# Kernel optimization log

Hardware: AMD Instinct MI355X
Metric: run time of the kernel (lower is better)

The kernel has to match this reference:

```python
import jax, jax.numpy as jnp
import numpy as np

DIM = 1024
N_HEADS = 16
HEAD_DIM = DIM // N_HEADS
COND_DIM = 1024
MLP_RATIO = 4
B = 8
L = 1024  # per-sequence length (equal lengths -> T = B*L packed tokens)
T = B * L
EPS = 1e-5


def setup_inputs() -> dict:
    key = jax.random.key(0)
    ks = jax.random.split(key, 16)
    s = 0.02
    # rotary tables: [max_pos, head_dim//2]
    inv_freq = 1.0 / (10000.0 ** (jnp.arange(0, HEAD_DIM, 2, dtype=jnp.float32) / HEAD_DIM))
    t = jnp.arange(L, dtype=jnp.float32)
    freqs = t[:, None] * inv_freq[None, :]  # [L, HEAD_DIM//2]
    return {
        "x": jax.random.normal(ks[0], (T, DIM), jnp.float32),
        "lengths": jnp.full((B,), L, dtype=jnp.int64),
        "offsets": jnp.arange(B, dtype=jnp.int64) * L,
        "cos": jnp.cos(freqs),
        "sin": jnp.sin(freqs),
        "positions": jnp.tile(jnp.arange(L, dtype=jnp.int64), B),
        "c": jax.random.normal(ks[1], (B, COND_DIM), jnp.float32),
        "ln1_w": jnp.ones((DIM,), jnp.float32),
        "Wq": jax.random.normal(ks[2], (DIM, DIM), jnp.float32) * s,
        "Wk": jax.random.normal(ks[3], (DIM, DIM), jnp.float32) * s,
        "Wv": jax.random.normal(ks[4], (DIM, DIM), jnp.float32) * s,
        "Wo": jax.random.normal(ks[5], (DIM, DIM), jnp.float32) * s,
        "ln2_w": jnp.ones((DIM,), jnp.float32),
        "W1": jax.random.normal(ks[6], (DIM, MLP_RATIO * DIM), jnp.float32) * s,
        "b1": jnp.zeros((MLP_RATIO * DIM,), jnp.float32),
        "W2": jax.random.normal(ks[7], (MLP_RATIO * DIM, DIM), jnp.float32) * s,
        "b2": jnp.zeros((DIM,), jnp.float32),
        "ada_w": jax.random.normal(ks[8], (COND_DIM, 6 * DIM), jnp.float32) * s,
        "ada_b": jnp.zeros((6 * DIM,), jnp.float32),
    }


def _layer_norm(x, w):
    # LayerNorm with weight only (no bias), as in the torch module
    mu = jnp.mean(x, axis=-1, keepdims=True)
    var = jnp.mean(jnp.square(x - mu), axis=-1, keepdims=True)
    return (x - mu) * jax.lax.rsqrt(var + EPS) * w


def _rope(q, k, cos, sin, positions):
    # q, k: [T, H, D]; cos/sin: [max_pos, D//2]; half-split RoPE
    c = cos[positions][:, None, :]  # [T, 1, D//2]
    s = sin[positions][:, None, :]
    def rot(x):
        x1, x2 = jnp.split(x, 2, axis=-1)
        return jnp.concatenate([x1 * c - x2 * s, x2 * c + x1 * s], axis=-1)
    return rot(q), rot(k)


def reference(x, lengths, offsets, cos, sin, positions, c,
              ln1_w, Wq, Wk, Wv, Wo, ln2_w, W1, b1, W2, b2, ada_w, ada_b):
    # adaLN modulation: [B, 6*DIM] -> six [B, DIM]
    ada = c @ ada_w + ada_b
    sh_msa, sc_msa, g_msa, sh_mlp, sc_mlp, g_mlp = jnp.split(ada, 6, axis=-1)
    # per-token gather via seq_ids (equal lengths -> repeat each row L times)
    seq_ids = jnp.repeat(jnp.arange(B), L)  # = repeat_interleave(arange(B), lengths)
    sh_msa_t, sc_msa_t, g_msa_t = sh_msa[seq_ids], sc_msa[seq_ids], g_msa[seq_ids]
    sh_mlp_t, sc_mlp_t, g_mlp_t = sh_mlp[seq_ids], sc_mlp[seq_ids], g_mlp[seq_ids]

    x_skip = x
    h = _layer_norm(x, ln1_w) * (1.0 + sc_msa_t) + sh_msa_t
    q = (h @ Wq).reshape(T, N_HEADS, HEAD_DIM)
    k = (h @ Wk).reshape(T, N_HEADS, HEAD_DIM)
    v = (h @ Wv).reshape(T, N_HEADS, HEAD_DIM)
    q, k = _rope(q, k, cos, sin, positions)

    # intra-sequence-only attention: with equal lengths the block-diagonal
    # score_mod mask is exactly per-sequence attention -> reshape to [B, L, H, D]
    qb = q.reshape(B, L, N_HEADS, HEAD_DIM)
    kb = k.reshape(B, L, N_HEADS, HEAD_DIM)
    vb = v.reshape(B, L, N_HEADS, HEAD_DIM)
    scores = jnp.einsum('blhd,bmhd->bhlm', qb, kb) / jnp.sqrt(jnp.float32(HEAD_DIM))
    probs = jax.nn.softmax(scores, axis=-1)
    attn = jnp.einsum('bhlm,bmhd->blhd', probs, vb).reshape(T, DIM)

    x = x_skip + g_msa_t * (attn @ Wo)  # dropout p is identity in eval mode

    h2 = _layer_norm(x, ln2_w) * (1.0 + sc_mlp_t) + sh_mlp_t
    mlp = jax.nn.gelu(h2 @ W1 + b1, approximate=True) @ W2 + b2
    return x + g_mlp_t * mlp
```

## Files before the change

kernel.cpp:

```cpp
#include <hip/hip_runtime.h>

typedef unsigned short u16;
typedef __attribute__((ext_vector_type(8))) short short8;
typedef __attribute__((ext_vector_type(4))) float f32x4;
typedef __attribute__((ext_vector_type(4))) unsigned uint4v;

__device__ __forceinline__ float bf2f(u16 u){
  unsigned v = ((unsigned)u) << 16;
  return __builtin_bit_cast(float, v);
}
__device__ __forceinline__ u16 f2bf(float f){
  unsigned u = __builtin_bit_cast(unsigned, f);
  u += 0x7fff + ((u >> 16) & 1);
  return (u16)(u >> 16);
}
__device__ __forceinline__ unsigned packbf(float lo, float hi){
  return ((unsigned)f2bf(hi) << 16) | (unsigned)f2bf(lo);
}
__device__ __forceinline__ void async16(const void* g, void* l){
  __builtin_amdgcn_global_load_lds((const __attribute__((address_space(1))) void*)g,
                                   (__attribute__((address_space(3))) void*)l, 16, 0, 0);
}
#define VMW(n) asm volatile("s_waitcnt vmcnt(" #n ")" ::: "memory")

__global__ __launch_bounds__(256) void ada_partial(
    const float* __restrict__ c, const float* __restrict__ aw,
    float* __restrict__ part){
  int n  = blockIdx.x*256 + threadIdx.x;
  int b  = blockIdx.y;
  int kc = blockIdx.z;
  const float* cr  = c + b*1024 + kc*128;
  const float* awp = aw + (size_t)(kc*128)*6144 + n;
  float acc = 0.f;
#pragma unroll 8
  for (int k = 0; k < 128; ++k)
    acc += cr[k] * awp[(size_t)k*6144];
  part[(size_t)(kc*8 + b)*6144 + n] = acc;
}

__global__ __launch_bounds__(256) void ada_reduce(
    const float* __restrict__ part, const float* __restrict__ ab,
    float* __restrict__ ada){
  int idx = blockIdx.x*256 + threadIdx.x;
  int n = idx % 6144;
  float acc = ab[n];
#pragma unroll
  for (int kc = 0; kc < 8; ++kc)
    acc += part[(size_t)kc*49152 + idx];
  ada[idx] = acc;
}

__global__ __launch_bounds__(256) void transpose_cast(
    const float* __restrict__ src, u16* __restrict__ dst, int K, int N){
  __shared__ float t[64][65];
  int n0 = blockIdx.x*64, k0 = blockIdx.y*64;
  int tid = threadIdx.x;
  int cc = tid & 63, r4 = tid >> 6;
#pragma unroll 4
  for (int it = 0; it < 16; ++it){
    int r = it*4 + r4;
    t[r][cc] = src[(size_t)(k0 + r)*N + n0 + cc];
  }
  __syncthreads();
#pragma unroll 4
  for (int it = 0; it < 16; ++it){
    int r = it*4 + r4;
    dst[(size_t)(n0 + r)*K + k0 + cc] = f2bf(t[cc][r]);
  }
}

__global__ __launch_bounds__(256) void ln_mod(
    const float* __restrict__ x, u16* __restrict__ out,
    const float* __restrict__ w, const float* __restrict__ ada,
    int shift_off, int scale_off){
  int t = blockIdx.x, tid = threadIdx.x;
  const float* xr = x + (size_t)t*1024;
  float v[4]; float s = 0.f, ss = 0.f;
#pragma unroll
  for (int i = 0; i < 4; ++i){ v[i] = xr[tid + i*256]; s += v[i]; ss += v[i]*v[i]; }
  for (int d = 1; d < 64; d <<= 1){ s += __shfl_xor(s, d); ss += __shfl_xor(ss, d); }
  __shared__ float red[8];
  int wv = tid >> 6;
  if ((tid & 63) == 0){ red[wv] = s; red[4+wv] = ss; }
  __syncthreads();
  s = red[0]+red[1]+red[2]+red[3];
  ss = red[4]+red[5]+red[6]+red[7];
  float mu = s * (1.f/1024.f);
  float var = ss * (1.f/1024.f) - mu*mu;
  float rs = rsqrtf(var + 1e-5f);
  int b = t >> 10;
  const float* sh = ada + b*6144 + shift_off;
  const float* sc = ada + b*6144 + scale_off;
#pragma unroll
  for (int i = 0; i < 4; ++i){
    int cidx = tid + i*256;
    float hh = (v[i]-mu)*rs*w[cidx]*(1.f + sc[cidx]) + sh[cidx];
    out[(size_t)t*1024 + cidx] = f2bf(hh);
  }
}

template<int EPI>
__device__ __forceinline__ void gemm_epi(
    void* Cout, int m, int n, int N, int m_off, float v,
    const float* e0, const float* e1, const float* e2){
  if (EPI == 0){
    ((u16*)Cout)[(size_t)m*N + n] = f2bf(v);
  } else if (EPI == 1){
    const int b = (m + m_off) >> 10;
    float g = e1[b*6144 + 2048 + n];
    ((float*)Cout)[(size_t)m*N + n] = e0[(size_t)m*N + n] + g*v;
  } else if (EPI == 2){
    float xx = v + e0[n];
    float u = xx*(1.5957691216f + 0.07135481626f*xx*xx);
    ((u16*)Cout)[(size_t)m*N + n] = f2bf(xx / (1.f + __expf(-u)));
  } else {
    const int b = (m + m_off) >> 10;
    float g = e1[b*6144 + 5120 + n];
    ((float*)Cout)[(size_t)m*N + n] = e2[(size_t)m*N + n] + g*(v + e0[n]);
  }
}

template<int EPI>
__global__ __launch_bounds__(512, 2) void gemm_bt(
    const u16* __restrict__ A, const u16* __restrict__ Bt,
    void* __restrict__ Cout, int M, int N, int K, int m_off,
    const float* __restrict__ e0, const float* __restrict__ e1,
    const float* __restrict__ e2){
  __shared__ u16 lds[65536];
  const int tid = threadIdx.x;
  const int wv = tid >> 6, lane = tid & 63;
  const int quad = lane >> 4, ln = lane & 15;
  const int wr = wv >> 2, wc = wv & 3;
  const int n0 = blockIdx.x*256, m0 = blockIdx.y*256;
  const int nt = K >> 5;

  const int swslot = (lane & 3) ^ ((lane >> 3) & 3);
  const u16* Ap = A  + (size_t)(m0 + wv*16 + (lane>>2))*K + swslot*8;
  const u16* Bp = Bt + (size_t)(n0 + wv*16 + (lane>>2))*K + swslot*8;
  const size_t hstep = (size_t)128*K;
  u16* lw = lds + wv*512;

  f32x4 acc[8][4] = {};

#pragma unroll
  for (int tau = 0; tau < 3; ++tau){
    u16* d = lw + tau*16384;
    async16(Ap + (size_t)tau*32,         d);
    async16(Ap + hstep + (size_t)tau*32, d + 4096);
    async16(Bp + (size_t)tau*32,         d + 8192);
    async16(Bp + hstep + (size_t)tau*32, d + 12288);
  }
  VMW(8);
  __builtin_amdgcn_s_barrier();

  const int rsw = (quad ^ ((ln >> 1) & 3))*8;
  const u16* Ar = lds + (wr*128 + ln)*32 + rsw;
  const u16* Br = lds + 8192 + (wc*64 + ln)*32 + rsw;

  for (int t = 0; t < nt; ++t){
    const int bo = (t & 3)*16384;
    short8 bfr[4], af[4];
#pragma unroll
    for (int j = 0; j < 4; ++j) bfr[j] = *(const short8*)(Br + bo + j*512);
#pragma unroll
    for (int i = 0; i < 4; ++i) af[i]  = *(const short8*)(Ar + bo + i*512);
    if (t + 3 < nt){
      u16* d = lw + ((t+3)&3)*16384;
      async16(Ap + (size_t)(t+3)*32,         d);
      async16(Ap + hstep + (size_t)(t+3)*32, d + 4096);
    }
    __builtin_amdgcn_s_barrier();
    __builtin_amdgcn_s_setprio(1);
#pragma unroll
    for (int i = 0; i < 4; ++i)
#pragma unroll
      for (int j = 0; j < 4; ++j)
        acc[i][j] = __builtin_amdgcn_mfma_f32_16x16x32_bf16(af[i], bfr[j], acc[i][j], 0, 0, 0);
    __builtin_amdgcn_s_setprio(0);
    __builtin_amdgcn_s_barrier();
#pragma unroll
    for (int i = 0; i < 4; ++i) af[i] = *(const short8*)(Ar + bo + 2048 + i*512);
    if (t + 3 < nt){
      u16* d = lw + ((t+3)&3)*16384;
      async16(Bp + (size_t)(t+3)*32,         d + 8192);
      async16(Bp + hstep + (size_t)(t+3)*32, d + 12288);
    }
    __builtin_amdgcn_s_barrier();
    __builtin_amdgcn_s_setprio(1);
#pragma unroll
    for (int i = 0; i < 4; ++i)
#pragma unroll
      for (int j = 0; j < 4; ++j)
        acc[4+i][j] = __builtin_amdgcn_mfma_f32_16x16x32_bf16(af[i], bfr[j], acc[4+i][j], 0, 0, 0);
    __builtin_amdgcn_s_setprio(0);
    if (t + 4 <= nt)      VMW(8);
    else if (t + 3 == nt) VMW(4);
    else if (t + 2 == nt) VMW(0);
    __builtin_amdgcn_s_barrier();
  }

  const int mB = m0 + wr*128 + quad*4;
  const int nB = n0 + wc*64 + ln;
#pragma unroll
  for (int i = 0; i < 8; ++i)
#pragma unroll
    for (int r = 0; r < 4; ++r)
#pragma unroll
      for (int j = 0; j < 4; ++j)
        gemm_epi<EPI>(Cout, mB + i*16 + r, nB + j*16, N, m_off, acc[i][j][r], e0, e1, e2);
}

template<int EPI>
__global__ __launch_bounds__(256, 2) void gemm_bt128(
    const u16* __restrict__ A, const u16* __restrict__ Bt,
    void* __restrict__ Cout, int M, int N, int K, int m_off,
    const float* __restrict__ e0, const float* __restrict__ e1,
    const float* __restrict__ e2){
  __shared__ u16 lds[32768];
  const int tid = threadIdx.x;
  const int wv = tid >> 6, lane = tid & 63;
  const int quad = lane >> 4, ln = lane & 15;
  const int wr = wv >> 1, wc = wv & 1;
  const int n0 = blockIdx.x*128, m0 = blockIdx.y*128;
  const int nt = K >> 5;

  const int swslot = (lane & 3) ^ ((lane >> 3) & 3);
  const u16* Ap = A  + (size_t)(m0 + wv*16 + (lane>>2))*K + swslot*8;
  const u16* Bp = Bt + (size_t)(n0 + wv*16 + (lane>>2))*K + swslot*8;
  const size_t hstep = (size_t)64*K;
  u16* lw = lds + wv*512;

  f32x4 acc[4][4] = {};

#pragma unroll
  for (int tau = 0; tau < 3; ++tau){
    u16* d = lw + tau*8192;
    async16(Ap + (size_t)tau*32,         d);
    async16(Ap + hstep + (size_t)tau*32, d + 2048);
    async16(Bp + (size_t)tau*32,         d + 4096);
    async16(Bp + hstep + (size_t)tau*32, d + 6144);
  }
  VMW(8);
  __builtin_amdgcn_s_barrier();

  const int rsw = (quad ^ ((ln >> 1) & 3))*8;
  const u16* Ar = lds + (wr*64 + ln)*32 + rsw;
  const u16* Br = lds + 4096 + (wc*64 + ln)*32 + rsw;

  for (int t = 0; t < nt; ++t){
    const int bo = (t & 3)*8192;
    short8 bfr[4], af[2];
#pragma unroll
    for (int j = 0; j < 4; ++j) bfr[j] = *(const short8*)(Br + bo + j*512);
#pragma unroll
    for (int i = 0; i < 2; ++i) af[i]  = *(const short8*)(Ar + bo + i*512);
    if (t + 3 < nt){
      u16* d = lw + ((t+3)&3)*8192;
      async16(Ap + (size_t)(t+3)*32,         d);
      async16(Ap + hstep + (size_t)(t+3)*32, d + 2048);
    }
    __builtin_amdgcn_s_barrier();
    __builtin_amdgcn_s_setprio(1);
#pragma unroll
    for (int i = 0; i < 2; ++i)
#pragma unroll
      for (int j = 0; j < 4; ++j)
        acc[i][j] = __builtin_amdgcn_mfma_f32_16x16x32_bf16(af[i], bfr[j], acc[i][j], 0, 0, 0);
    __builtin_amdgcn_s_setprio(0);
    __builtin_amdgcn_s_barrier();
#pragma unroll
    for (int i = 0; i < 2; ++i) af[i] = *(const short8*)(Ar + bo + 1024 + i*512);
    if (t + 3 < nt){
      u16* d = lw + ((t+3)&3)*8192;
      async16(Bp + (size_t)(t+3)*32,         d + 4096);
      async16(Bp + hstep + (size_t)(t+3)*32, d + 6144);
    }
    __builtin_amdgcn_s_barrier();
    __builtin_amdgcn_s_setprio(1);
#pragma unroll
    for (int i = 0; i < 2; ++i)
#pragma unroll
      for (int j = 0; j < 4; ++j)
        acc[2+i][j] = __builtin_amdgcn_mfma_f32_16x16x32_bf16(af[i], bfr[j], acc[2+i][j], 0, 0, 0);
    __builtin_amdgcn_s_setprio(0);
    if (t + 4 <= nt)      VMW(8);
    else if (t + 3 == nt) VMW(4);
    else if (t + 2 == nt) VMW(0);
    __builtin_amdgcn_s_barrier();
  }

  const int mB = m0 + wr*64 + quad*4;
  const int nB = n0 + wc*64 + ln;
#pragma unroll
  for (int i = 0; i < 4; ++i)
#pragma unroll
    for (int r = 0; r < 4; ++r)
#pragma unroll
      for (int j = 0; j < 4; ++j)
        gemm_epi<EPI>(Cout, mB + i*16 + r, nB + j*16, N, m_off, acc[i][j][r], e0, e1, e2);
}

__global__ __launch_bounds__(256) void rope_pack(
    const u16* __restrict__ qkv, const float* __restrict__ cosT,
    const float* __restrict__ sinT, u16* __restrict__ qp,
    u16* __restrict__ kp, u16* __restrict__ vt){
  int blk = blockIdx.x;
  int lt = blk & 15, h = (blk >> 4) & 15, b = blk >> 8;
  int l0 = lt*64;
  int bh = b*16 + h;
  __shared__ u16 vl[64][68];
  int tid = threadIdx.x;
  size_t tile_base = (size_t)bh*65536 + (size_t)lt*4096;
#pragma unroll 4
  for (int it = 0; it < 16; ++it){
    int idx = it*256 + tid;
    int r = idx >> 6, d = idx & 63;
    int t = b*1024 + l0 + r;
    int pos = l0 + r;
    const u16* row = qkv + (size_t)t*3072 + h*64;
    float qv = bf2f(row[d]), kv = bf2f(row[1024+d]);
    float qo, ko;
    if (d < 32){
      float cs = cosT[pos*32 + d], sn = sinT[pos*32 + d];
      qo = qv*cs - bf2f(row[d+32])*sn;
      ko = kv*cs - bf2f(row[1024+d+32])*sn;
    } else {
      int dd = d - 32;
      float cs = cosT[pos*32 + dd], sn = sinT[pos*32 + dd];
      qo = qv*cs + bf2f(row[d-32])*sn;
      ko = kv*cs + bf2f(row[1024+d-32])*sn;
    }
    qp[((size_t)bh*1024 + l0 + r)*64 + d] = f2bf(qo*0.125f);
    kp[tile_base + (d>>5)*2048 + r*32 + (d&31)] = f2bf(ko);
    vl[d][r] = row[2048 + d];
  }
  __syncthreads();
#pragma unroll 4
  for (int it = 0; it < 16; ++it){
    int idx = it*256 + tid;
    int d = idx >> 6, cc = idx & 63;
    vt[tile_base + (cc>>5)*2048 + d*32 + (cc&31)] = vl[d][cc];
  }
}

__global__ __launch_bounds__(256) void attn_kernel(
    const u16* __restrict__ qp, const u16* __restrict__ kp,
    const u16* __restrict__ vtp, u16* __restrict__ ao){
  __shared__ u16 Kb[4096];
  __shared__ u16 Vb[4096];
  int tid = threadIdx.x, w = tid >> 6, lane = tid & 63;
  int quad = lane >> 4, ln = lane & 15;
  int bh = blockIdx.x >> 4, qb = blockIdx.x & 15;
  int h = bh & 15, b = bh >> 4;
  const u16* Q  = qp  + ((size_t)bh*1024 + qb*64 + w*16)*64;
  const u16* Kg = kp  + (size_t)bh*65536;
  const u16* Vg = vtp + (size_t)bh*65536;
  short8 qf0 = *(const short8*)(Q + ln*64 + quad*8);
  short8 qf1 = *(const short8*)(Q + ln*64 + 32 + quad*8);
  f32x4 o[4] = {};
  float m = -3e38f, l = 0.f;
  for (int kt = 0; kt < 16; ++kt){
    const u16* ktg = Kg + kt*4096 + lane*8;
    const u16* vtg = Vg + kt*4096 + lane*8;
    async16(ktg + (w*2+0)*512, Kb + (w*2+0)*512);
    async16(ktg + (w*2+1)*512, Kb + (w*2+1)*512);
    async16(vtg + (w*2+0)*512, Vb + (w*2+0)*512);
    async16(vtg + (w*2+1)*512, Vb + (w*2+1)*512);
    __syncthreads();
    f32x4 zz = {0.f, 0.f, 0.f, 0.f};
    f32x4 st[4];
#pragma unroll
    for (int c = 0; c < 4; ++c){
      short8 k0 = *(const short8*)(Kb +        (c*16 + ln)*32 + quad*8);
      short8 k1 = *(const short8*)(Kb + 2048 + (c*16 + ln)*32 + quad*8);
      st[c] = __builtin_amdgcn_mfma_f32_16x16x32_bf16(k0, qf0, zz, 0,0,0);
      st[c] = __builtin_amdgcn_mfma_f32_16x16x32_bf16(k1, qf1, st[c], 0,0,0);
    }
    short8 va[4][2];
#pragma unroll
    for (int dc = 0; dc < 4; ++dc)
#pragma unroll
      for (int kh = 0; kh < 2; ++kh)
        va[dc][kh] = *(const short8*)(Vb + kh*2048 + (dc*16 + ln)*32 + quad*8);
    float mx = st[0][0];
#pragma unroll
    for (int c = 0; c < 4; ++c)
#pragma unroll
      for (int r = 0; r < 4; ++r) mx = fmaxf(mx, st[c][r]);
    mx = fmaxf(mx, __shfl_xor(mx, 16));
    mx = fmaxf(mx, __shfl_xor(mx, 32));
    float mn = fmaxf(m, mx);
    float alpha = __expf(m - mn);
    m = mn;
    float p[4][4];
#pragma unroll
    for (int c = 0; c < 4; ++c)
#pragma unroll
      for (int r = 0; r < 4; ++r) p[c][r] = __expf(st[c][r] - mn);
    float sum = ((p[0][0]+p[0][1]) + (p[0][2]+p[0][3])) + ((p[1][0]+p[1][1]) + (p[1][2]+p[1][3]))
              + ((p[2][0]+p[2][1]) + (p[2][2]+p[2][3])) + ((p[3][0]+p[3][1]) + (p[3][2]+p[3][3]));
    sum += __shfl_xor(sum, 16);
    sum += __shfl_xor(sum, 32);
    l = l*alpha + sum;
#pragma unroll
    for (int dc = 0; dc < 4; ++dc)
#pragma unroll
      for (int r = 0; r < 4; ++r) o[dc][r] *= alpha;
    unsigned pc[4][2];
#pragma unroll
    for (int c = 0; c < 4; ++c){
      pc[c][0] = packbf(p[c][0], p[c][1]);
      pc[c][1] = packbf(p[c][2], p[c][3]);
    }
    const int sA = ((quad & 1)*2)*16 + ln;
    const int sB = sA + 16;
    const bool hi = quad >= 2;
#pragma unroll
    for (int kh = 0; kh < 2; ++kh){
      unsigned a0 = (unsigned)__shfl((int)pc[2*kh][0],   sA);
      unsigned b0 = (unsigned)__shfl((int)pc[2*kh+1][0], sA);
      unsigned a1 = (unsigned)__shfl((int)pc[2*kh][1],   sA);
      unsigned b1 = (unsigned)__shfl((int)pc[2*kh+1][1], sA);
      unsigned a2 = (unsigned)__shfl((int)pc[2*kh][0],   sB);
      unsigned b2 = (unsigned)__shfl((int)pc[2*kh+1][0], sB);
      unsigned a3 = (unsigned)__shfl((int)pc[2*kh][1],   sB);
      unsigned b3 = (unsigned)__shfl((int)pc[2*kh+1][1], sB);
      uint4v u = { hi ? b0 : a0, hi ? b1 : a1, hi ? b2 : a2, hi ? b3 : a3 };
      short8 pfrag = __builtin_bit_cast(short8, u);
#pragma unroll
      for (int dc = 0; dc < 4; ++dc)
        o[dc] = __builtin_amdgcn_mfma_f32_16x16x32_bf16(va[dc][kh], pfrag, o[dc], 0,0,0);
    }
    __syncthreads();
  }
  float rl = 1.f / l;
  size_t orow = ((size_t)b*1024 + qb*64 + w*16 + ln)*1024 + h*64;
#pragma unroll
  for (int dc = 0; dc < 4; ++dc)
#pragma unroll
    for (int r = 0; r < 4; ++r)
      ao[orow + dc*16 + quad*4 + r] = f2bf(o[dc][r] * rl);
}

extern "C" void kernel_launch(void* const* d_in, const int* in_sizes, int n_in,
                              void* d_out, int out_size, void* d_ws, size_t ws_size,
                              hipStream_t stream){
  const float* x    = (const float*)d_in[0];
  const float* cosT = (const float*)d_in[3];
  const float* sinT = (const float*)d_in[4];
  const float* c    = (const float*)d_in[6];
  const float* ln1w = (const float*)d_in[7];
  const float* Wq   = (const float*)d_in[8];
  const float* Wk   = (const float*)d_in[9];
  const float* Wv   = (const float*)d_in[10];
  const float* Wo   = (const float*)d_in[11];
  const float* ln2w = (const float*)d_in[12];
  const float* W1   = (const float*)d_in[13];
  const float* b1   = (const float*)d_in[14];
  const float* W2   = (const float*)d_in[15];
  const float* b2   = (const float*)d_in[16];
  const float* adaW = (const float*)d_in[17];
  const float* adaB = (const float*)d_in[18];

  char* ws = (char*)d_ws;
  float* ada  = (float*)(ws);
  u16* wqkvt  = (u16*)  (ws + 262144);
  u16* wot    = (u16*)  (ws + 6553600);
  u16* w1t    = (u16*)  (ws + 8650752);
  u16* w2t    = (u16*)  (ws + 17039360);
  u16* h      = (u16*)  (ws + 25427968);
  u16* qp     = (u16*)  (ws + 25427968);
  u16* h2     = (u16*)  (ws + 25427968);
  u16* qkv    = (u16*)  (ws + 42205184);
  u16* attnb  = (u16*)  (ws + 42205184);
  float* xmid = (float*)(ws + 58982400);
  float* adaP = (float*)(ws + 92536832);
  u16* kp     = (u16*)  (ws + 92536832);
  u16* vt     = (u16*)  (ws + 109314048);
  u16* hid    = (u16*)  (ws + 92536832);
  u16* hidF   = (u16*)  (ws + 126091264);
  float* out  = (float*)d_out;
  const bool bigws = ws_size >= (size_t)193200128;

  ada_partial<<<dim3(24,8,8), 256, 0, stream>>>(c, adaW, adaP);
  ada_reduce<<<192, 256, 0, stream>>>(adaP, adaB, ada);
  transpose_cast<<<dim3(16,16), 256, 0, stream>>>(Wq, wqkvt,             1024, 1024);
  transpose_cast<<<dim3(16,16), 256, 0, stream>>>(Wk, wqkvt + 1024*1024, 1024, 1024);
  transpose_cast<<<dim3(16,16), 256, 0, stream>>>(Wv, wqkvt + 2048*1024, 1024, 1024);
  transpose_cast<<<dim3(16,16), 256, 0, stream>>>(Wo, wot,               1024, 1024);
  transpose_cast<<<dim3(64,16), 256, 0, stream>>>(W1, w1t,               1024, 4096);
  transpose_cast<<<dim3(16,64), 256, 0, stream>>>(W2, w2t,               4096, 1024);
  ln_mod<<<8192, 256, 0, stream>>>(x, h, ln1w, ada, 0, 1024);
  gemm_bt128<0><<<dim3(24,64), 256, 0, stream>>>(h, wqkvt, qkv, 8192, 3072, 1024, 0,
                                                 nullptr, nullptr, nullptr);
  rope_pack<<<2048, 256, 0, stream>>>(qkv, cosT, sinT, qp, kp, vt);
  attn_kernel<<<2048, 256, 0, stream>>>(qp, kp, vt, attnb);
  gemm_bt128<1><<<dim3(8,64), 256, 0, stream>>>(attnb, wot, xmid, 8192, 1024, 1024, 0,
                                                x, ada, nullptr);
  ln_mod<<<8192, 256, 0, stream>>>(xmid, h2, ln2w, ada, 3072, 4096);
  if (bigws){
    gemm_bt<2><<<dim3(16,32), 512, 0, stream>>>(h2, w1t, hidF, 8192, 4096, 1024, 0,
                                                b1, nullptr, nullptr);
    gemm_bt128<3><<<dim3(8,64), 256, 0, stream>>>(hidF, w2t, out, 8192, 1024, 4096, 0,
                                                  b2, ada, xmid);
  } else {
    for (int cch = 0; cch < 2; ++cch){
      const size_t mo = (size_t)cch*4096;
      gemm_bt<2><<<dim3(16,16), 512, 0, stream>>>(h2 + mo*1024, w1t, hid,
                                                  4096, 4096, 1024, (int)mo,
                                                  b1, nullptr, nullptr);
      gemm_bt128<3><<<dim3(8,32), 256, 0, stream>>>(hid, w2t, out + mo*1024,
                                                    4096, 1024, 4096, (int)mo,
                                                    b2, ada, xmid + mo*1024);
    }
  }
}
```

Baseline: 601.6 us.

## Double-buffer attention K/V tiles, swizzle LDS layout, add lazy softmax rescale

The attention kernel now double-buffers K and V tiles in LDS, prefetching the next tile with async global-to-LDS loads while the current tile is computed, and uses explicit vmcnt waits with raw barriers in place of __syncthreads. The K/V layout written by the prep kernel is XOR-swizzled so that the LDS fragment reads avoid bank conflicts. Softmax rescaling of o and l is skipped unless the running max grows by more than 8, MFMA sections get raised wave priority, and the block index mapping is reordered so that blocks sharing a head are spread apart. The cost is double the LDS use, and the lazy rescale lets exponentials reach up to e^8 before renormalising, which is a small numerical risk.

```diff
diff --git a/kernel.cpp b/kernel.cpp
--- a/kernel.cpp
+++ b/kernel.cpp
@@ -331,7 +331,8 @@
       ko = kv*cs + bf2f(row[1024+d-32])*sn;
     }
     qp[((size_t)bh*1024 + l0 + r)*64 + d] = f2bf(qo*0.125f);
-    kp[tile_base + (d>>5)*2048 + r*32 + (d&31)] = f2bf(ko);
+    int ksl = ((d&31) >> 3) ^ ((r >> 1) & 3);
+    kp[tile_base + (d>>5)*2048 + r*32 + (ksl<<3) + (d&7)] = f2bf(ko);
     vl[d][r] = row[2048 + d];
   }
   __syncthreads();
@@ -339,49 +340,65 @@
   for (int it = 0; it < 16; ++it){
     int idx = it*256 + tid;
     int d = idx >> 6, cc = idx & 63;
-    vt[tile_base + (cc>>5)*2048 + d*32 + (cc&31)] = vl[d][cc];
+    int vsl = ((cc&31) >> 3) ^ ((d >> 1) & 3);
+    vt[tile_base + (cc>>5)*2048 + d*32 + (vsl<<3) + (cc&7)] = vl[d][cc];
   }
 }
 
 __global__ __launch_bounds__(256) void attn_kernel(
     const u16* __restrict__ qp, const u16* __restrict__ kp,
     const u16* __restrict__ vtp, u16* __restrict__ ao){
-  __shared__ u16 Kb[4096];
-  __shared__ u16 Vb[4096];
+  __shared__ u16 Kb[2][4096];
+  __shared__ u16 Vb[2][4096];
   int tid = threadIdx.x, w = tid >> 6, lane = tid & 63;
   int quad = lane >> 4, ln = lane & 15;
-  int bh = blockIdx.x >> 4, qb = blockIdx.x & 15;
+  int bh = blockIdx.x & 127, qb = blockIdx.x >> 7;
   int h = bh & 15, b = bh >> 4;
   const u16* Q  = qp  + ((size_t)bh*1024 + qb*64 + w*16)*64;
-  const u16* Kg = kp  + (size_t)bh*65536;
-  const u16* Vg = vtp + (size_t)bh*65536;
+  const u16* Kg = kp  + (size_t)bh*65536 + lane*8;
+  const u16* Vg = vtp + (size_t)bh*65536 + lane*8;
   short8 qf0 = *(const short8*)(Q + ln*64 + quad*8);
   short8 qf1 = *(const short8*)(Q + ln*64 + 32 + quad*8);
   f32x4 o[4] = {};
   float m = -3e38f, l = 0.f;
+  const int rsw = (quad ^ ((ln >> 1) & 3))*8;
+
+  async16(Kg + (w*2+0)*512, Kb[0] + (w*2+0)*512);
+  async16(Kg + (w*2+1)*512, Kb[0] + (w*2+1)*512);
+  async16(Vg + (w*2+0)*512, Vb[0] + (w*2+0)*512);
+  async16(Vg + (w*2+1)*512, Vb[0] + (w*2+1)*512);
+
   for (int kt = 0; kt < 16; ++kt){
-    const u16* ktg = Kg + kt*4096 + lane*8;
-    const u16* vtg = Vg + kt*4096 + lane*8;
-    async16(ktg + (w*2+0)*512, Kb + (w*2+0)*512);
-    async16(ktg + (w*2+1)*512, Kb + (w*2+1)*512);
-    async16(vtg + (w*2+0)*512, Vb + (w*2+0)*512);
-    async16(vtg + (w*2+1)*512, Vb + (w*2+1)*512);
-    __syncthreads();
+    const int cur = kt & 1;
+    if (kt < 15){
+      const u16* ktg = Kg + (kt+1)*4096;
+      const u16* vtg = Vg + (kt+1)*4096;
+      async16(ktg + (w*2+0)*512, Kb[cur^1] + (w*2+0)*512);
+      async16(ktg + (w*2+1)*512, Kb[cur^1] + (w*2+1)*512);
+      async16(vtg + (w*2+0)*512, Vb[cur^1] + (w*2+0)*512);
+      async16(vtg + (w*2+1)*512, Vb[cur^1] + (w*2+1)*512);
+      VMW(4);
+    } else {
+      VMW(0);
+    }
+    __builtin_amdgcn_s_barrier();
     f32x4 zz = {0.f, 0.f, 0.f, 0.f};
     f32x4 st[4];
+    __builtin_amdgcn_s_setprio(1);
 #pragma unroll
     for (int c = 0; c < 4; ++c){
-      short8 k0 = *(const short8*)(Kb +        (c*16 + ln)*32 + quad*8);
-      short8 k1 = *(const short8*)(Kb + 2048 + (c*16 + ln)*32 + quad*8);
+      short8 k0 = *(const short8*)(Kb[cur] +        (c*16 + ln)*32 + rsw);
+      short8 k1 = *(const short8*)(Kb[cur] + 2048 + (c*16 + ln)*32 + rsw);
       st[c] = __builtin_amdgcn_mfma_f32_16x16x32_bf16(k0, qf0, zz, 0,0,0);
       st[c] = __builtin_amdgcn_mfma_f32_16x16x32_bf16(k1, qf1, st[c], 0,0,0);
     }
+    __builtin_amdgcn_s_setprio(0);
     short8 va[4][2];
 #pragma unroll
     for (int dc = 0; dc < 4; ++dc)
 #pragma unroll
       for (int kh = 0; kh < 2; ++kh)
-        va[dc][kh] = *(const short8*)(Vb + kh*2048 + (dc*16 + ln)*32 + quad*8);
+        va[dc][kh] = *(const short8*)(Vb[cur] + kh*2048 + (dc*16 + ln)*32 + rsw);
     float mx = st[0][0];
 #pragma unroll
     for (int c = 0; c < 4; ++c)
@@ -389,23 +406,26 @@
       for (int r = 0; r < 4; ++r) mx = fmaxf(mx, st[c][r]);
     mx = fmaxf(mx, __shfl_xor(mx, 16));
     mx = fmaxf(mx, __shfl_xor(mx, 32));
-    float mn = fmaxf(m, mx);
-    float alpha = __expf(m - mn);
-    m = mn;
+    if (__any(mx > m + 8.f)){
+      float mn = fmaxf(m, mx);
+      float alpha = __expf(m - mn);
+      m = mn;
+      l *= alpha;
+#pragma unroll
+      for (int dc = 0; dc < 4; ++dc)
+#pragma unroll
+        for (int r = 0; r < 4; ++r) o[dc][r] *= alpha;
+    }
     float p[4][4];
 #pragma unroll
     for (int c = 0; c < 4; ++c)
 #pragma unroll
-      for (int r = 0; r < 4; ++r) p[c][r] = __expf(st[c][r] - mn);
+      for (int r = 0; r < 4; ++r) p[c][r] = __expf(st[c][r] - m);
     float sum = ((p[0][0]+p[0][1]) + (p[0][2]+p[0][3])) + ((p[1][0]+p[1][1]) + (p[1][2]+p[1][3]))
               + ((p[2][0]+p[2][1]) + (p[2][2]+p[2][3])) + ((p[3][0]+p[3][1]) + (p[3][2]+p[3][3]));
     sum += __shfl_xor(sum, 16);
     sum += __shfl_xor(sum, 32);
-    l = l*alpha + sum;
-#pragma unroll
-    for (int dc = 0; dc < 4; ++dc)
-#pragma unroll
-      for (int r = 0; r < 4; ++r) o[dc][r] *= alpha;
+    l += sum;
     unsigned pc[4][2];
 #pragma unroll
     for (int c = 0; c < 4; ++c){
@@ -427,11 +447,13 @@
       unsigned b3 = (unsigned)__shfl((int)pc[2*kh+1][1], sB);
       uint4v u = { hi ? b0 : a0, hi ? b1 : a1, hi ? b2 : a2, hi ? b3 : a3 };
       short8 pfrag = __builtin_bit_cast(short8, u);
+      __builtin_amdgcn_s_setprio(1);
 #pragma unroll
       for (int dc = 0; dc < 4; ++dc)
         o[dc] = __builtin_amdgcn_mfma_f32_16x16x32_bf16(va[dc][kh], pfrag, o[dc], 0,0,0);
-    }
-    __syncthreads();
+      __builtin_amdgcn_s_setprio(0);
+    }
+    __builtin_amdgcn_s_barrier();
   }
   float rl = 1.f / l;
   size_t orow = ((size_t)b*1024 + qb*64 + w*16 + ln)*1024 + h*64;
```

Result: no change. 605.9 us (+0.7%).
